# Optimization experiments

Hardware: AMD Instinct MI355X
Metric: run time of the kernel (lower is better)

Reference implementation:

```python
import jax, jax.numpy as jnp
import numpy as np

B, K, NPROP, NSAMPLE = 16, 2048, 256, 16
C_SEED, C_MLP = 256, 128
RADIUS = 0.3
NH, NSC, NCLS = 12, 18, 18
KZ, KXY, KLINE = 1024, 1024, 1024
SURF_TH, UP_TH = 0.5, 10.0
OUT_CH = 2 + 3 + 2 * NH + 4 * NSC + NCLS  # 119


def setup_inputs():
    key = jax.random.key(0)
    ks = iter(jax.random.split(key, 64))
    nrm = lambda shape, sc=1.0: sc * jax.random.normal(next(ks), shape, jnp.float32)
    uni = lambda shape: jax.random.uniform(next(ks), shape, jnp.float32, minval=-2.0, maxval=2.0)
    inp = {
        'vote_xyz': uni((B, K, 3)),
        'vote_features': nrm((B, C_SEED, K)),
        'pred_sem_class_z': nrm((B, 2, KZ)),
        'center_z': uni((B, KZ, 3)),
        'aggregated_feature_z': nrm((B, 128, KZ)),
        'pred_sem_class_xy': nrm((B, 2, KXY)),
        'center_xy': uni((B, KXY, 3)),
        'aggregated_feature_xy': nrm((B, 128, KXY)),
        'pred_sem_class_line': nrm((B, 2, KLINE)),
        'center_line': uni((B, KLINE, 3)),
        'aggregated_feature_line': nrm((B, 128, KLINE)),
        'mean_size_arr': jnp.abs(nrm((NSC, 3))) * 0.5 + 0.3,
        'mlp_w0': nrm((C_MLP, C_SEED + 3), 0.05),
        'mlp_s0': 1.0 + nrm((C_MLP,), 0.02),
        'mlp_b0': nrm((C_MLP,), 0.02),
        'mlp_w1': nrm((C_MLP, C_MLP), 0.05),
        'mlp_s1': 1.0 + nrm((C_MLP,), 0.02),
        'mlp_b1': nrm((C_MLP,), 0.02),
        'mlp_w2': nrm((C_MLP, C_MLP), 0.05),
        'mlp_s2': 1.0 + nrm((C_MLP,), 0.02),
        'mlp_b2': nrm((C_MLP,), 0.02),
        'conv1_w': nrm((C_MLP, C_MLP), 0.05),
        'conv1_b': nrm((C_MLP,), 0.02),
        'bn1_s': 1.0 + nrm((C_MLP,), 0.02),
        'bn1_b': nrm((C_MLP,), 0.02),
        'conv2_w': nrm((C_MLP, C_MLP), 0.05),
        'conv2_b': nrm((C_MLP,), 0.02),
        'bn2_s': 1.0 + nrm((C_MLP,), 0.02),
        'bn2_b': nrm((C_MLP,), 0.02),
        'conv3_w': nrm((OUT_CH, C_MLP), 0.05),
        'conv3_b': nrm((OUT_CH,), 0.02),
    }
    return inp


def fps(xyz, npoint):
    # furthest point sampling; xyz (B,N,3) -> (B,npoint) int32
    Bn, N, _ = xyz.shape
    bidx = jnp.arange(Bn)

    def step(carry, _):
        dist, far = carry
        centroid = xyz[bidx, far][:, None, :]  # (B,1,3)
        d = jnp.sum((xyz - centroid) ** 2, -1)
        dist = jnp.minimum(dist, d)
        nxt = jnp.argmax(dist, -1).astype(jnp.int32)
        return (dist, nxt), far

    init = (jnp.full((Bn, N), 1e10, xyz.dtype), jnp.zeros((Bn,), jnp.int32))
    _, inds = jax.lax.scan(step, init, None, length=npoint)
    return inds.T


def ball_group(xyz, feat_t, new_xyz, radius, nsample):
    # first-nsample-in-ball semantics (as CUDA ball_query), pad with first hit
    Bn, N, _ = xyz.shape
    d2 = jnp.sum((new_xyz[:, :, None] - xyz[:, None]) ** 2, -1)  # (B,P,N)
    score = jnp.where(d2 <= radius * radius, jnp.arange(N, dtype=jnp.int32), N)
    neg, idx = jax.lax.top_k(-score, nsample)
    idx = jnp.where(-neg < N, idx, idx[..., :1])
    b = jnp.arange(Bn)[:, None, None]
    gx = (xyz[b, idx] - new_xyz[:, :, None]) / radius  # normalize_xyz=True
    gf = feat_t[b, idx]
    return jnp.concatenate([gx, gf], -1)  # (B,P,ns,3+C)


def reference(vote_xyz, vote_features, pred_sem_class_z, center_z, aggregated_feature_z,
              pred_sem_class_xy, center_xy, aggregated_feature_xy,
              pred_sem_class_line, center_line, aggregated_feature_line, mean_size_arr,
              mlp_w0, mlp_s0, mlp_b0, mlp_w1, mlp_s1, mlp_b1, mlp_w2, mlp_s2, mlp_b2,
              conv1_w, conv1_b, bn1_s, bn1_b, conv2_w, conv2_b, bn2_s, bn2_b, conv3_w, conv3_b):
    # --- vote aggregation (PointnetSAModuleVotes, vote_fps) ---
    fps_inds = fps(vote_xyz, NPROP)
    bi = jnp.arange(vote_xyz.shape[0])[:, None]
    new_xyz = vote_xyz[bi, fps_inds]  # (B,P,3)
    g = ball_group(vote_xyz, vote_features.transpose(0, 2, 1), new_xyz, RADIUS, NSAMPLE)
    for w, s, b in ((mlp_w0, mlp_s0, mlp_b0), (mlp_w1, mlp_s1, mlp_b1), (mlp_w2, mlp_s2, mlp_b2)):
        g = jax.nn.relu(jnp.einsum('bpsc,oc->bpso', g, w) * s + b)  # conv2d 1x1 + folded BN + relu
    features = g.max(axis=2).transpose(0, 2, 1)  # (B,128,P)

    c1d = lambda x, w, b: jnp.einsum('bck,oc->bok', x, w) + b[None, :, None]
    bn = lambda x, s, b: x * s[None, :, None] + b[None, :, None]

    net = jax.nn.relu(bn(c1d(features, conv1_w, conv1_b), bn1_s, bn1_b))
    net = jax.nn.relu(bn(c1d(net, conv2_w, conv2_b), bn2_s, bn2_b))
    net = c1d(net, conv3_w, conv3_b)  # (B,119,P)

    # --- decode_scores (mode='center', start=2) ---
    nt = net.transpose(0, 2, 1)
    Bn, P = nt.shape[0], nt.shape[1]
    objectness = nt[..., 0:2]
    center = new_xyz + nt[..., 2:5]
    heading_scores = nt[..., 5:5 + NH]
    heading_res = nt[..., 5 + NH:5 + 2 * NH] * (np.pi / NH)
    size_scores = nt[..., 5 + 2 * NH:5 + 2 * NH + NSC]
    srn = nt[..., 5 + 2 * NH + NSC:5 + 2 * NH + 4 * NSC].reshape(Bn, P, NSC, 3)
    size_res = srn * mean_size_arr[None, None]
    sem_cls = nt[..., 5 + 2 * NH + 4 * NSC:]

    # --- surface / line center selection ---
    def sel_center(pred_sem, c):
        p = jax.nn.softmax(pred_sem, axis=1)
        sel = jax.lax.stop_gradient((p[:, 1, :] <= SURF_TH).astype(c.dtype))
        return c + UP_TH * sel[..., None]

    z_center = sel_center(pred_sem_class_z, center_z)
    xy_center = sel_center(pred_sem_class_xy, center_xy)
    line_center = sel_center(pred_sem_class_line, center_line)
    surface_center_pred = jnp.concatenate([z_center, xy_center], axis=1)
    surface_center_feature_pred = jnp.concatenate([aggregated_feature_z, aggregated_feature_xy], axis=2)

    # --- predicted box size -> 6 object surface centers ---
    cls = jnp.argmax(size_scores, -1)  # (B,P)
    pred_res = jnp.take_along_axis(size_res, cls[..., None, None], axis=2)[:, :, 0]
    pred_avg = mean_size_arr[cls]
    obj_size = jax.lax.stop_gradient(pred_avg + pred_res)  # .detach() in torch
    half = obj_size / 2.0
    z0 = jnp.zeros_like(half[..., :1])
    ez = jnp.concatenate([z0, z0, half[..., 2:3]], -1)
    ey = jnp.concatenate([z0, half[..., 1:2], z0], -1)
    ex = jnp.concatenate([half[..., 0:1], z0, z0], -1)
    obj_surface_center = jnp.concatenate([center + ez, center - ez, center + ey,
                                          center - ey, center + ex, center - ex], axis=1)
    obj_surface_feature = jnp.tile(features, (1, 1, 6))

    return (objectness, center, heading_scores, heading_res, size_scores, size_res, sem_cls,
            surface_center_pred, surface_center_feature_pred, line_center,
            obj_surface_center, obj_surface_feature)
```

## Files before the change

### kernel.cpp

```cpp
#include <hip/hip_runtime.h>

#define BB 16
#define KK 2048
#define NPROPN 256
#define NS 16
#define CSEED 256
#define CMLP 128
#define CIN 259
#define OUTCH 119
#define KZZ 1024

#define O0  0UL
#define O1  8192UL
#define O2  20480UL
#define O3  69632UL
#define O4  118784UL
#define O5  192512UL
#define O6  413696UL
#define O7  487424UL
#define O8  585728UL
#define O9  4780032UL
#define O10 4829184UL
#define O11 4902912UL

#define WS_NEWXYZ 0
#define WS_W0T 12288
#define WS_W1T 45440
#define WS_W2T 61824
#define WS_C1T 78208
#define WS_C2T 94592
#define WS_C3T 110976
#define WS_FEATT 131072UL
#define WS_NEED_BYTES ((size_t)(WS_FEATT + (size_t)BB * KK * CSEED) * 4)

#define XROWS 131
#define XSTR (XROWS * 16)

#define RSTEP(CTRL)                                                                          \
  {                                                                                          \
    unsigned shi = (unsigned)__builtin_amdgcn_update_dpp((int)hi, (int)hi, (CTRL), 0xF, 0xF, false); \
    unsigned slo = (unsigned)__builtin_amdgcn_update_dpp((int)lo, (int)lo, (CTRL), 0xF, 0xF, false); \
    bool gt = (shi > hi) || ((shi == hi) && (slo > lo));                                     \
    hi = gt ? shi : hi;                                                                      \
    lo = gt ? slo : lo;                                                                      \
  }

__device__ __forceinline__ void fma4(float4& a, float s, const float4& w) {
  a.x = fmaf(s, w.x, a.x); a.y = fmaf(s, w.y, a.y);
  a.z = fmaf(s, w.z, a.z); a.w = fmaf(s, w.w, a.w);
}
__device__ __forceinline__ float fget(const float4& v, int r) {
  return r == 0 ? v.x : (r == 1 ? v.y : (r == 2 ? v.z : v.w));
}
__device__ __forceinline__ int xadr(int row, int s4) {
  return row * 16 + (((s4) ^ ((row >> 2) & 3)) << 2);
}

template<bool TR>
__global__ __launch_bounds__(256) void prep_kernel(
    const float* __restrict__ xyz, const float* __restrict__ vote_feat,
    const float* __restrict__ w0, const float* __restrict__ w1, const float* __restrict__ w2,
    const float* __restrict__ c1w, const float* __restrict__ c2w, const float* __restrict__ c3w,
    const float* __restrict__ pz, const float* __restrict__ cz,
    const float* __restrict__ pxy, const float* __restrict__ cxy,
    const float* __restrict__ pl, const float* __restrict__ cl,
    const float* __restrict__ az, const float* __restrict__ axy,
    float* __restrict__ wsf, float* __restrict__ out) {
  constexpr int FPS_END = 16;
  constexpr int FEATT_END = FPS_END + (TR ? 1024 : 0);
  constexpr int TRW_END = FEATT_END + 450;
  constexpr int SURF_END = TRW_END + 192;

  const int bid = blockIdx.x;
  const int t = threadIdx.x;
  __shared__ float smem[8448];
  __shared__ unsigned fhi[2][4], flo[2][4];

  if (bid < FPS_END) {
    const int b = bid;
    const float* p = xyz + (size_t)b * KK * 3;
    float* sxyz = smem;
    float* nxb = smem + 6144;
    const int lane = t & 63, w = t >> 6;
    float pxr[8], pyr[8], pzr[8], dd[8];
#pragma unroll
    for (int j = 0; j < 8; ++j) {
      int i = j * 256 + t;
      float x = p[i * 3 + 0], y = p[i * 3 + 1], z = p[i * 3 + 2];
      pxr[j] = x; pyr[j] = y; pzr[j] = z; dd[j] = 1e10f;
      sxyz[i * 3 + 0] = x; sxyz[i * 3 + 1] = y; sxyz[i * 3 + 2] = z;
    }
    __syncthreads();
    int cur = 0;
    for (int it = 0; it < NPROPN; ++it) {
      const int pb = it & 1;
      float cx = sxyz[cur * 3 + 0];
      float cy = sxyz[cur * 3 + 1];
      float cz2 = sxyz[cur * 3 + 2];
      if (t == 0) { nxb[it * 3 + 0] = cx; nxb[it * 3 + 1] = cy; nxb[it * 3 + 2] = cz2; }
      float best = -1.0f;
      int bidx = 0;
#pragma unroll
      for (int j = 0; j < 8; ++j) {
        float dx = __fsub_rn(pxr[j], cx);
        float dy = __fsub_rn(pyr[j], cy);
        float dz = __fsub_rn(pzr[j], cz2);
        float d = __fadd_rn(__fadd_rn(__fmul_rn(dx, dx), __fmul_rn(dy, dy)), __fmul_rn(dz, dz));
        float nd = fminf(dd[j], d);
        dd[j] = nd;
        if (nd > best) { best = nd; bidx = j * 256 + t; }
      }
      unsigned hi = __float_as_uint(best);
      unsigned lo = ~(unsigned)bidx;
      RSTEP(0x111) RSTEP(0x112) RSTEP(0x114) RSTEP(0x118)
      RSTEP(0x142) RSTEP(0x143)
      if (lane == 63) { fhi[pb][w] = hi; flo[pb][w] = lo; }
      __syncthreads();
      unsigned vh = fhi[pb][0], vl = flo[pb][0];
#pragma unroll
      for (int q2 = 1; q2 < 4; ++q2) {
        unsigned ah = fhi[pb][q2], al = flo[pb][q2];
        bool gt = (ah > vh) || ((ah == vh) && (al > vl));
        vh = gt ? ah : vh; vl = gt ? al : vl;
      }
      cur = (int)~vl;
    }
    __syncthreads();
    float* nxw = wsf + WS_NEWXYZ + (size_t)b * NPROPN * 3;
    for (int i = t; i < NPROPN * 3; i += 256) nxw[i] = nxb[i];
    return;
  }

  if (TR && bid < FEATT_END) {
    int q = bid - FPS_END;
    int b = q >> 6, ck = q & 63;
    int k0 = ck << 5;
    float* tile = smem;
    const float* src = vote_feat + ((size_t)b * CSEED + t) * KK + k0;
    float4 v[8];
#pragma unroll
    for (int j = 0; j < 8; ++j) v[j] = *(const float4*)(src + j * 4);
#pragma unroll
    for (int j = 0; j < 8; ++j) {
      tile[(j * 4 + 0) * 260 + t] = v[j].x;
      tile[(j * 4 + 1) * 260 + t] = v[j].y;
      tile[(j * 4 + 2) * 260 + t] = v[j].z;
      tile[(j * 4 + 3) * 260 + t] = v[j].w;
    }
    __syncthreads();
    float* dst = wsf + WS_FEATT + ((size_t)b * KK + k0) * CSEED;
    const int kk = t >> 3, cbase = (t & 7) << 2;
#pragma unroll
    for (int j = 0; j < 8; ++j) {
      int c = cbase + (j << 5);
      float4 u = make_float4(tile[kk * 260 + c], tile[kk * 260 + c + 1],
                             tile[kk * 260 + c + 2], tile[kk * 260 + c + 3]);
      *(float4*)(dst + (size_t)kk * CSEED + c) = u;
    }
    return;
  }

  if (bid < TRW_END) {
    int row = (bid - FEATT_END) * 2 + (t >> 7);
    int o = t & 127;
    if (row < 899) {
      float v; float* dst;
      if (row < 259)      { dst = wsf + WS_W0T + (size_t)row * 128; v = w0[(size_t)o * CIN + row]; }
      else if (row < 387) { int k = row - 259; dst = wsf + WS_W1T + (size_t)k * 128; v = w1[(size_t)o * 128 + k]; }
      else if (row < 515) { int k = row - 387; dst = wsf + WS_W2T + (size_t)k * 128; v = w2[(size_t)o * 128 + k]; }
      else if (row < 643) { int k = row - 515; dst = wsf + WS_C1T + (size_t)k * 128; v = c1w[(size_t)o * 128 + k]; }
      else if (row < 771) { int k = row - 643; dst = wsf + WS_C2T + (size_t)k * 128; v = c2w[(size_t)o * 128 + k]; }
      else                { int k = row - 771; dst = wsf + WS_C3T + (size_t)k * 128; v = (o < OUTCH) ? c3w[(size_t)o * 128 + k] : 0.f; }
      dst[o] = v;
    }
    return;
  }

  if (bid < SURF_END) {
    int i = (bid - TRW_END) * 256 + t;
    int src = i / (BB * KZZ);
    int rem = i % (BB * KZZ);
    int b = rem / KZZ, k = rem % KZZ;
    const float* ps = (src == 0) ? pz : ((src == 1) ? pxy : pl);
    const float* pc = (src == 0) ? cz : ((src == 1) ? cxy : cl);
    float x0 = ps[((size_t)b * 2 + 0) * KZZ + k];
    float x1 = ps[((size_t)b * 2 + 1) * KZZ + k];
    float add = (x1 <= x0) ? 10.0f : 0.0f;
    size_t dst;
    if (src == 0)      dst = O7 + ((size_t)b * 2048 + k) * 3;
    else if (src == 1) dst = O7 + ((size_t)b * 2048 + 1024 + k) * 3;
    else               dst = O9 + ((size_t)b * KZZ + k) * 3;
    const float* c3 = pc + ((size_t)b * KZZ + k) * 3;
    out[dst + 0] = c3[0] + add;
    out[dst + 1] = c3[1] + add;
    out[dst + 2] = c3[2] + add;
    return;
  }

  {
    int i = (bid - SURF_END) * 256 + t;
    int q = i & 511;
    int bc = i >> 9;
    int half = q >> 8, k4 = q & 255;
    const float4* src = (const float4*)((half == 0) ? az : axy);
    float4 v = src[(size_t)bc * 256 + k4];
    float4* dst = (float4*)(out + O8);
    dst[(size_t)bc * 512 + q] = v;
  }
}

__device__ __forceinline__ void mlp_accum(const float* __restrict__ WT, int og, int sh,
                                          const float* __restrict__ xb, int K, float4* acc) {
  const float4* wp = (const float4*)WT + og;
  const int s4a = sh * 2, s4b = sh * 2 + 1;
#pragma unroll 4
  for (int k = 0; k < K; ++k) {
    float4 xa = *(const float4*)(xb + xadr(k, s4a));
    float4 xq = *(const float4*)(xb + xadr(k, s4b));
    float4 wv = wp[(size_t)k * 32];
    fma4(acc[0], xa.x, wv); fma4(acc[1], xa.y, wv);
    fma4(acc[2], xa.z, wv); fma4(acc[3], xa.w, wv);
    fma4(acc[4], xq.x, wv); fma4(acc[5], xq.y, wv);
    fma4(acc[6], xq.z, wv); fma4(acc[7], xq.w, wv);
  }
}

__device__ __forceinline__ void mlp_storeh(const float* __restrict__ scv, const float* __restrict__ bbv,
                                           int og, int sh, float* __restrict__ xb,
                                           const float4* __restrict__ acc) {
  float4 s4v = *(const float4*)(scv + (og << 2));
  float4 b4v = *(const float4*)(bbv + (og << 2));
#pragma unroll
  for (int r = 0; r < 4; ++r) {
    float ss = fget(s4v, r), bv = fget(b4v, r);
    float4 lo, hi;
    lo.x = fmaf(fget(acc[0], r), ss, bv); lo.x = lo.x > 0.f ? lo.x : 0.f;
    lo.y = fmaf(fget(acc[1], r), ss, bv); lo.y = lo.y > 0.f ? lo.y : 0.f;
    lo.z = fmaf(fget(acc[2], r), ss, bv); lo.z = lo.z > 0.f ? lo.z : 0.f;
    lo.w = fmaf(fget(acc[3], r), ss, bv); lo.w = lo.w > 0.f ? lo.w : 0.f;
    hi.x = fmaf(fget(acc[4], r), ss, bv); hi.x = hi.x > 0.f ? hi.x : 0.f;
    hi.y = fmaf(fget(acc[5], r), ss, bv); hi.y = hi.y > 0.f ? hi.y : 0.f;
    hi.z = fmaf(fget(acc[6], r), ss, bv); hi.z = hi.z > 0.f ? hi.z : 0.f;
    hi.w = fmaf(fget(acc[7], r), ss, bv); hi.w = hi.w > 0.f ? hi.w : 0.f;
    int row = (og << 2) + r;
    *(float4*)(xb + xadr(row, sh * 2)) = lo;
    *(float4*)(xb + xadr(row, sh * 2 + 1)) = hi;
  }
}

template<bool TR>
__global__ __launch_bounds__(256, 3) void proposal_kernel(
    const float* __restrict__ vote_xyz, const float* __restrict__ vote_feat,
    const float* __restrict__ wsf, const float* __restrict__ msa,
    const float* __restrict__ s0, const float* __restrict__ b0,
    const float* __restrict__ s1, const float* __restrict__ b1,
    const float* __restrict__ s2, const float* __restrict__ b2,
    const float* __restrict__ c1b, const float* __restrict__ bn1s, const float* __restrict__ bn1b,
    const float* __restrict__ c2b, const float* __restrict__ bn2s, const float* __restrict__ bn2b,
    const float* __restrict__ c3b,
    float* __restrict__ out) {
  __shared__ __align__(16) float Xbuf[4 * XSTR];
  __shared__ int sel_s[4][NS];
  __shared__ float feat_s[4][CMLP];
  __shared__ float n1_s[4][CMLP], n2_s[4][CMLP], ntv_s[4][CMLP];
  __shared__ float sc_s[4][3], sh_s[4][3];
  __shared__ int scls_s[4];

  const int t = threadIdx.x;
  const int w = t >> 6, l = t & 63;
  const int b = blockIdx.x >> 6;
  const int pp = ((blockIdx.x & 63) << 2) + w;
  const int sh = l >> 5, og = l & 31;
  float* Xw = Xbuf + w * XSTR;

  const float* nx = wsf + WS_NEWXYZ + ((size_t)b * NPROPN + pp) * 3;
  const float cx = nx[0], cy = nx[1], cz = nx[2];
  const float* px = vote_xyz + (size_t)b * KK * 3;
  const float RR = 0.09000000357627869f;

  {
    int total = 0;
    for (int j = 0; j < 32; ++j) {
      int i = (j << 6) + l;
      float dx = __fsub_rn(px[i * 3 + 0], cx);
      float dy = __fsub_rn(px[i * 3 + 1], cy);
      float dz = __fsub_rn(px[i * 3 + 2], cz);
      float d = __fadd_rn(__fadd_rn(__fmul_rn(dx, dx), __fmul_rn(dy, dy)), __fmul_rn(dz, dz));
      bool in = (d <= RR);
      unsigned long long bal = __ballot(in);
      if (in) {
        int pos = total + __popcll(bal & ((1ull << l) - 1ull));
        if (pos < NS) sel_s[w][pos] = i;
      }
      total += __popcll(bal);
      if (total >= NS) break;
    }
    if (l == 0 && total < NS) {
      int first = (total > 0) ? sel_s[w][0] : 0;
      for (int i = total; i < NS; ++i) sel_s[w][i] = first;
    }
    __builtin_amdgcn_wave_barrier();
  }

  float4 pf[8];
  {
    const int s = l >> 2, q = l & 3;
    const int idx = sel_s[w][s];
    const int s4 = s >> 2, se = s & 3;
    if (q < 3) {
      float pv = px[idx * 3 + q];
      float cv = (q == 0) ? cx : ((q == 1) ? cy : cz);
      Xw[xadr(q, s4) + se] = __fdiv_rn(__fsub_rn(pv, cv), 0.3f);
    }
    if constexpr (TR) {
      const float* fr = wsf + WS_FEATT + ((size_t)b * KK + idx) * CSEED;
#pragma unroll
      for (int m = 0; m < 8; ++m) {
        int c = (m << 4) + (q << 2);
        float4 v = *(const float4*)(fr + c);
        Xw[xadr(3 + c + 0, s4) + se] = v.x;
        Xw[xadr(3 + c + 1, s4) + se] = v.y;
        Xw[xadr(3 + c + 2, s4) + se] = v.z;
        Xw[xadr(3 + c + 3, s4) + se] = v.w;
      }
#pragma unroll
      for (int m = 0; m < 8; ++m) pf[m] = *(const float4*)(fr + 128 + (m << 4) + (q << 2));
    } else {
      const float* fb = vote_feat + (size_t)b * CSEED * KK + idx;
#pragma unroll
      for (int m = 0; m < 8; ++m) {
        int c = (m << 4) + (q << 2);
        Xw[xadr(3 + c + 0, s4) + se] = fb[(size_t)(c + 0) * KK];
        Xw[xadr(3 + c + 1, s4) + se] = fb[(size_t)(c + 1) * KK];
        Xw[xadr(3 + c + 2, s4) + se] = fb[(size_t)(c + 2) * KK];
        Xw[xadr(3 + c + 3, s4) + se] = fb[(size_t)(c + 3) * KK];
      }
#pragma unroll
      for (int m = 0; m < 8; ++m) {
        int c = 128 + (m << 4) + (q << 2);
        pf[m].x = fb[(size_t)(c + 0) * KK];
        pf[m].y = fb[(size_t)(c + 1) * KK];
        pf[m].z = fb[(size_t)(c + 2) * KK];
        pf[m].w = fb[(size_t)(c + 3) * KK];
      }
    }
    __builtin_amdgcn_wave_barrier();
  }

  float4 acc[8];
#pragma unroll
  for (int i = 0; i < 8; ++i) acc[i] = make_float4(0.f, 0.f, 0.f, 0.f);

  mlp_accum(wsf + WS_W0T, og, sh, Xw, 131, acc);
  __builtin_amdgcn_wave_barrier();

  {
    const int s = l >> 2, q = l & 3;
    const int s4 = s >> 2, se = s & 3;
#pragma unroll
    for (int m = 0; m < 8; ++m) {
      int c = (m << 4) + (q << 2);
      Xw[xadr(c + 0, s4) + se] = pf[m].x;
      Xw[xadr(c + 1, s4) + se] = pf[m].y;
      Xw[xadr(c + 2, s4) + se] = pf[m].z;
      Xw[xadr(c + 3, s4) + se] = pf[m].w;
    }
    __builtin_amdgcn_wave_barrier();
  }

  mlp_accum(wsf + WS_W0T + 131 * 128, og, sh, Xw, 128, acc);
  mlp_storeh(s0, b0, og, sh, Xw, acc);
  __builtin_amdgcn_wave_barrier();

#pragma unroll
  for (int i = 0; i < 8; ++i) acc[i] = make_float4(0.f, 0.f, 0.f, 0.f);
  mlp_accum(wsf + WS_W1T, og, sh, Xw, 128, acc);
  mlp_storeh(s1, b1, og, sh, Xw, acc);
  __builtin_amdgcn_wave_barrier();

#pragma unroll
  for (int i = 0; i < 8; ++i) acc[i] = make_float4(0.f, 0.f, 0.f, 0.f);
  mlp_accum(wsf + WS_W2T, og, sh, Xw, 128, acc);

  float mr[4];
  {
    float4 s4v = *(const float4*)(s2 + (og << 2));
    float4 b4v = *(const float4*)(b2 + (og << 2));
#pragma unroll
    for (int r = 0; r < 4; ++r) {
      float ss = fget(s4v, r), bv = fget(b4v, r);
      float m = 0.f;
#pragma unroll
      for (int i = 0; i < 8; ++i) m = fmaxf(m, fmaf(fget(acc[i], r), ss, bv));
      mr[r] = fmaxf(m, __shfl_xor(m, 32));
    }
  }
  if (sh == 0) *(float4*)&feat_s[w][og << 2] = make_float4(mr[0], mr[1], mr[2], mr[3]);
  __builtin_amdgcn_wave_barrier();

  {
    float* o11 = out + O11 + (size_t)b * CMLP * 1536;
#pragma unroll
    for (int r = 0; r < 4; ++r) {
      size_t rowb = (size_t)((og << 2) + r) * 1536 + pp;
#pragma unroll
      for (int rr2 = 0; rr2 < 3; ++rr2) {
        int rr = sh * 3 + rr2;
        o11[rowb + rr * 256] = mr[r];
      }
    }
  }

  {
    const float* C1T = wsf + WS_C1T;
    float a0 = 0.f, a1 = 0.f;
#pragma unroll 4
    for (int k = 0; k < CMLP; ++k) {
      float f = feat_s[w][k];
      float2 wv = *(const float2*)(C1T + (size_t)k * 128 + (l << 1));
      a0 = fmaf(f, wv.x, a0); a1 = fmaf(f, wv.y, a1);
    }
    int o0 = l << 1, o1 = o0 + 1;
    float v0 = fmaf(a0 + c1b[o0], bn1s[o0], bn1b[o0]); v0 = v0 > 0.f ? v0 : 0.f;
    float v1 = fmaf(a1 + c1b[o1], bn1s[o1], bn1b[o1]); v1 = v1 > 0.f ? v1 : 0.f;
    *(float2*)&n1_s[w][o0] = make_float2(v0, v1);
    __builtin_amdgcn_wave_barrier();
  }
  {
    const float* C2T = wsf + WS_C2T;
    float a0 = 0.f, a1 = 0.f;
#pragma unroll 4
    for (int k = 0; k < CMLP; ++k) {
      float f = n1_s[w][k];
      float2 wv = *(const float2*)(C2T + (size_t)k * 128 + (l << 1));
      a0 = fmaf(f, wv.x, a0); a1 = fmaf(f, wv.y, a1);
    }
    int o0 = l << 1, o1 = o0 + 1;
    float v0 = fmaf(a0 + c2b[o0], bn2s[o0], bn2b[o0]); v0 = v0 > 0.f ? v0 : 0.f;
    float v1 = fmaf(a1 + c2b[o1], bn2s[o1], bn2b[o1]); v1 = v1 > 0.f ? v1 : 0.f;
    *(float2*)&n2_s[w][o0] = make_float2(v0, v1);
    __builtin_amdgcn_wave_barrier();
  }
  {
    const float* C3T = wsf + WS_C3T;
    float a0 = 0.f, a1 = 0.f;
#pragma unroll 4
    for (int k = 0; k < CMLP; ++k) {
      float f = n2_s[w][k];
      float2 wv = *(const float2*)(C3T + (size_t)k * 128 + (l << 1));
      a0 = fmaf(f, wv.x, a0); a1 = fmaf(f, wv.y, a1);
    }
    int o0 = l << 1, o1 = o0 + 1;
    float bb0 = (o0 < OUTCH) ? c3b[o0] : 0.f;
    float bb1 = (o1 < OUTCH) ? c3b[o1] : 0.f;
    *(float2*)&ntv_s[w][o0] = make_float2(a0 + bb0, a1 + bb1);
    __builtin_amdgcn_wave_barrier();
  }

  {
    const float* ntv = &ntv_s[w][0];
    const size_t bp = (size_t)b * NPROPN + pp;
    if (l < 2) out[O0 + bp * 2 + l] = ntv[l];
    if (l < 3) {
      float cv = ((l == 0) ? cx : ((l == 1) ? cy : cz)) + ntv[2 + l];
      sc_s[w][l] = cv;
      out[O1 + bp * 3 + l] = cv;
    }
    if (l < 12) {
      out[O2 + bp * 12 + l] = ntv[5 + l];
      out[O3 + bp * 12 + l] = ntv[17 + l] * 0.2617993877991494f;
    }
    if (l < 18) {
      out[O4 + bp * 18 + l] = ntv[29 + l];
      out[O6 + bp * 18 + l] = ntv[101 + l];
    }
    if (l < 54) out[O5 + bp * 54 + l] = ntv[47 + l] * msa[l];
    if (l == 0) {
      float bvv = ntv[29]; int bii = 0;
      for (int i2 = 1; i2 < 18; ++i2)
        if (ntv[29 + i2] > bvv) { bvv = ntv[29 + i2]; bii = i2; }
      scls_s[w] = bii;
    }
    __builtin_amdgcn_wave_barrier();
    if (l < 3) {
      int cls = scls_s[w];
      float m = msa[cls * 3 + l];
      sh_s[w][l] = fmaf(ntv[47 + cls * 3 + l], m, m) * 0.5f;
    }
    __builtin_amdgcn_wave_barrier();
    if (l < 18) {
      const int r = l / 3, j2 = l % 3;
      const int axis[6] = {2, 2, 1, 1, 0, 0};
      float v = sc_s[w][j2];
      if (j2 == axis[r]) v = (r & 1) ? (v - sh_s[w][j2]) : (v + sh_s[w][j2]);
      out[O10 + (size_t)b * 4608 + (size_t)(r * 256 + pp) * 3 + j2] = v;
    }
  }
}

extern "C" void kernel_launch(void* const* d_in, const int* in_sizes, int n_in,
                              void* d_out, int out_size, void* d_ws, size_t ws_size,
                              hipStream_t stream) {
  (void)in_sizes; (void)n_in; (void)out_size;
  const float* vote_xyz = (const float*)d_in[0];
  const float* vote_feat = (const float*)d_in[1];
  const float* pz   = (const float*)d_in[2];
  const float* cz   = (const float*)d_in[3];
  const float* az   = (const float*)d_in[4];
  const float* pxy  = (const float*)d_in[5];
  const float* cxy  = (const float*)d_in[6];
  const float* axy  = (const float*)d_in[7];
  const float* pl   = (const float*)d_in[8];
  const float* cl   = (const float*)d_in[9];
  const float* msa  = (const float*)d_in[11];
  const float* w0   = (const float*)d_in[12];
  const float* s0   = (const float*)d_in[13];
  const float* b0   = (const float*)d_in[14];
  const float* w1   = (const float*)d_in[15];
  const float* s1   = (const float*)d_in[16];
  const float* b1   = (const float*)d_in[17];
  const float* w2   = (const float*)d_in[18];
  const float* s2   = (const float*)d_in[19];
  const float* b2   = (const float*)d_in[20];
  const float* c1w  = (const float*)d_in[21];
  const float* c1b  = (const float*)d_in[22];
  const float* bn1s = (const float*)d_in[23];
  const float* bn1b = (const float*)d_in[24];
  const float* c2w  = (const float*)d_in[25];
  const float* c2b  = (const float*)d_in[26];
  const float* bn2s = (const float*)d_in[27];
  const float* bn2b = (const float*)d_in[28];
  const float* c3w  = (const float*)d_in[29];
  const float* c3b  = (const float*)d_in[30];
  float* out = (float*)d_out;
  float* wsf = (float*)d_ws;

  if (ws_size >= WS_NEED_BYTES) {
    hipLaunchKernelGGL((prep_kernel<true>), dim3(16 + 1024 + 450 + 192 + 4096), dim3(256), 0, stream,
                       vote_xyz, vote_feat, w0, w1, w2, c1w, c2w, c3w,
                       pz, cz, pxy, cxy, pl, cl, az, axy, wsf, out);
    hipLaunchKernelGGL((proposal_kernel<true>), dim3(BB * NPROPN / 4), dim3(256), 0, stream,
                       vote_xyz, vote_feat, wsf, msa,
                       s0, b0, s1, b1, s2, b2,
                       c1b, bn1s, bn1b, c2b, bn2s, bn2b, c3b, out);
  } else {
    hipLaunchKernelGGL((prep_kernel<false>), dim3(16 + 450 + 192 + 4096), dim3(256), 0, stream,
                       vote_xyz, vote_feat, w0, w1, w2, c1w, c2w, c3w,
                       pz, cz, pxy, cxy, pl, cl, az, axy, wsf, out);
    hipLaunchKernelGGL((proposal_kernel<false>), dim3(BB * NPROPN / 4), dim3(256), 0, stream,
                       vote_xyz, vote_feat, wsf, msa,
                       s0, b0, s1, b1, s2, b2,
                       c1b, bn1s, bn1b, c2b, bn2s, bn2b, c3b, out);
  }
}
```

Baseline: 377.3 us.

## Carry FPS winner coordinates through DPP reduction and alias proposal scratch into Xbuf

Measured after the change: 379.9 us. Within noise of the previous version (+0.7%).

```diff
diff --git a/kernel.cpp b/kernel.cpp
--- a/kernel.cpp
+++ b/kernel.cpp
@@ -36,13 +36,16 @@
 #define XROWS 131
 #define XSTR (XROWS * 16)
 
-#define RSTEP(CTRL)                                                                          \
-  {                                                                                          \
+#define RSTEP5(CTRL)                                                                           \
+  {                                                                                            \
     unsigned shi = (unsigned)__builtin_amdgcn_update_dpp((int)hi, (int)hi, (CTRL), 0xF, 0xF, false); \
     unsigned slo = (unsigned)__builtin_amdgcn_update_dpp((int)lo, (int)lo, (CTRL), 0xF, 0xF, false); \
-    bool gt = (shi > hi) || ((shi == hi) && (slo > lo));                                     \
-    hi = gt ? shi : hi;                                                                      \
-    lo = gt ? slo : lo;                                                                      \
+    unsigned sx  = (unsigned)__builtin_amdgcn_update_dpp((int)bx, (int)bx, (CTRL), 0xF, 0xF, false); \
+    unsigned sy  = (unsigned)__builtin_amdgcn_update_dpp((int)by, (int)by, (CTRL), 0xF, 0xF, false); \
+    unsigned sz  = (unsigned)__builtin_amdgcn_update_dpp((int)bz, (int)bz, (CTRL), 0xF, 0xF, false); \
+    bool gt = (shi > hi) || ((shi == hi) && (slo > lo));                                       \
+    hi = gt ? shi : hi; lo = gt ? slo : lo;                                                    \
+    bx = gt ? sx : bx;  by = gt ? sy : by;  bz = gt ? sz : bz;                                 \
   }
 
 __device__ __forceinline__ void fma4(float4& a, float s, const float4& w) {
@@ -74,56 +77,67 @@
   const int bid = blockIdx.x;
   const int t = threadIdx.x;
   __shared__ float smem[8448];
-  __shared__ unsigned fhi[2][4], flo[2][4];
+  __shared__ __align__(16) unsigned fres[2][5][4];
 
   if (bid < FPS_END) {
     const int b = bid;
     const float* p = xyz + (size_t)b * KK * 3;
-    float* sxyz = smem;
-    float* nxb = smem + 6144;
+    float* nxb = smem;
     const int lane = t & 63, w = t >> 6;
     float pxr[8], pyr[8], pzr[8], dd[8];
 #pragma unroll
     for (int j = 0; j < 8; ++j) {
       int i = j * 256 + t;
-      float x = p[i * 3 + 0], y = p[i * 3 + 1], z = p[i * 3 + 2];
-      pxr[j] = x; pyr[j] = y; pzr[j] = z; dd[j] = 1e10f;
-      sxyz[i * 3 + 0] = x; sxyz[i * 3 + 1] = y; sxyz[i * 3 + 2] = z;
-    }
-    __syncthreads();
-    int cur = 0;
+      pxr[j] = p[i * 3 + 0]; pyr[j] = p[i * 3 + 1]; pzr[j] = p[i * 3 + 2];
+      dd[j] = 1e10f;
+    }
+    float ccx = p[0], ccy = p[1], ccz = p[2];
     for (int it = 0; it < NPROPN; ++it) {
       const int pb = it & 1;
-      float cx = sxyz[cur * 3 + 0];
-      float cy = sxyz[cur * 3 + 1];
-      float cz2 = sxyz[cur * 3 + 2];
-      if (t == 0) { nxb[it * 3 + 0] = cx; nxb[it * 3 + 1] = cy; nxb[it * 3 + 2] = cz2; }
+      if (t == 0) { nxb[it * 3 + 0] = ccx; nxb[it * 3 + 1] = ccy; nxb[it * 3 + 2] = ccz; }
       float best = -1.0f;
-      int bidx = 0;
+      int bj = 0;
 #pragma unroll
       for (int j = 0; j < 8; ++j) {
-        float dx = __fsub_rn(pxr[j], cx);
-        float dy = __fsub_rn(pyr[j], cy);
-        float dz = __fsub_rn(pzr[j], cz2);
+        float dx = __fsub_rn(pxr[j], ccx);
+        float dy = __fsub_rn(pyr[j], ccy);
+        float dz = __fsub_rn(pzr[j], ccz);
         float d = __fadd_rn(__fadd_rn(__fmul_rn(dx, dx), __fmul_rn(dy, dy)), __fmul_rn(dz, dz));
         float nd = fminf(dd[j], d);
         dd[j] = nd;
-        if (nd > best) { best = nd; bidx = j * 256 + t; }
+        if (nd > best) { best = nd; bj = j; }
+      }
+      float fx = pxr[0], fy = pyr[0], fz = pzr[0];
+#pragma unroll
+      for (int j = 1; j < 8; ++j) {
+        bool e = (bj == j);
+        fx = e ? pxr[j] : fx; fy = e ? pyr[j] : fy; fz = e ? pzr[j] : fz;
       }
       unsigned hi = __float_as_uint(best);
-      unsigned lo = ~(unsigned)bidx;
-      RSTEP(0x111) RSTEP(0x112) RSTEP(0x114) RSTEP(0x118)
-      RSTEP(0x142) RSTEP(0x143)
-      if (lane == 63) { fhi[pb][w] = hi; flo[pb][w] = lo; }
+      unsigned lo = ~(unsigned)((bj << 8) + t);
+      unsigned bx = __float_as_uint(fx), by = __float_as_uint(fy), bz = __float_as_uint(fz);
+      RSTEP5(0x111) RSTEP5(0x112) RSTEP5(0x114) RSTEP5(0x118)
+      RSTEP5(0x142) RSTEP5(0x143)
+      if (lane == 63) {
+        fres[pb][0][w] = hi; fres[pb][1][w] = lo;
+        fres[pb][2][w] = bx; fres[pb][3][w] = by; fres[pb][4][w] = bz;
+      }
       __syncthreads();
-      unsigned vh = fhi[pb][0], vl = flo[pb][0];
-#pragma unroll
-      for (int q2 = 1; q2 < 4; ++q2) {
-        unsigned ah = fhi[pb][q2], al = flo[pb][q2];
-        bool gt = (ah > vh) || ((ah == vh) && (al > vl));
-        vh = gt ? ah : vh; vl = gt ? al : vl;
-      }
-      cur = (int)~vl;
+      uint4 H = *(const uint4*)&fres[pb][0][0];
+      uint4 L = *(const uint4*)&fres[pb][1][0];
+      uint4 X = *(const uint4*)&fres[pb][2][0];
+      uint4 Y = *(const uint4*)&fres[pb][3][0];
+      uint4 Z = *(const uint4*)&fres[pb][4][0];
+      unsigned vh = H.x, vl = L.x, vx = X.x, vy = Y.x, vz = Z.x;
+      {
+        bool g1 = (H.y > vh) || ((H.y == vh) && (L.y > vl));
+        vh = g1 ? H.y : vh; vl = g1 ? L.y : vl; vx = g1 ? X.y : vx; vy = g1 ? Y.y : vy; vz = g1 ? Z.y : vz;
+        bool g2 = (H.z > vh) || ((H.z == vh) && (L.z > vl));
+        vh = g2 ? H.z : vh; vl = g2 ? L.z : vl; vx = g2 ? X.z : vx; vy = g2 ? Y.z : vy; vz = g2 ? Z.z : vz;
+        bool g3 = (H.w > vh) || ((H.w == vh) && (L.w > vl));
+        vh = g3 ? H.w : vh; vl = g3 ? L.w : vl; vx = g3 ? X.w : vx; vy = g3 ? Y.w : vy; vz = g3 ? Z.w : vz;
+      }
+      ccx = __uint_as_float(vx); ccy = __uint_as_float(vy); ccz = __uint_as_float(vz);
     }
     __syncthreads();
     float* nxw = wsf + WS_NEWXYZ + (size_t)b * NPROPN * 3;
@@ -249,7 +263,7 @@
 }
 
 template<bool TR>
-__global__ __launch_bounds__(256, 3) void proposal_kernel(
+__global__ __launch_bounds__(256, 4) void proposal_kernel(
     const float* __restrict__ vote_xyz, const float* __restrict__ vote_feat,
     const float* __restrict__ wsf, const float* __restrict__ msa,
     const float* __restrict__ s0, const float* __restrict__ b0,
@@ -261,8 +275,6 @@
     float* __restrict__ out) {
   __shared__ __align__(16) float Xbuf[4 * XSTR];
   __shared__ int sel_s[4][NS];
-  __shared__ float feat_s[4][CMLP];
-  __shared__ float n1_s[4][CMLP], n2_s[4][CMLP], ntv_s[4][CMLP];
   __shared__ float sc_s[4][3], sh_s[4][3];
   __shared__ int scls_s[4];
 
@@ -272,6 +284,10 @@
   const int pp = ((blockIdx.x & 63) << 2) + w;
   const int sh = l >> 5, og = l & 31;
   float* Xw = Xbuf + w * XSTR;
+  float* feat_p = Xw;
+  float* n1_p   = Xw + 128;
+  float* n2_p   = Xw + 256;
+  float* ntv_p  = Xw + 384;
 
   const float* nx = wsf + WS_NEWXYZ + ((size_t)b * NPROPN + pp) * 3;
   const float cx = nx[0], cy = nx[1], cz = nx[2];
@@ -395,7 +411,8 @@
       mr[r] = fmaxf(m, __shfl_xor(m, 32));
     }
   }
-  if (sh == 0) *(float4*)&feat_s[w][og << 2] = make_float4(mr[0], mr[1], mr[2], mr[3]);
+  __builtin_amdgcn_wave_barrier();
+  if (sh == 0) *(float4*)(feat_p + (og << 2)) = make_float4(mr[0], mr[1], mr[2], mr[3]);
   __builtin_amdgcn_wave_barrier();
 
   {
@@ -416,14 +433,14 @@
     float a0 = 0.f, a1 = 0.f;
 #pragma unroll 4
     for (int k = 0; k < CMLP; ++k) {
-      float f = feat_s[w][k];
+      float f = feat_p[k];
       float2 wv = *(const float2*)(C1T + (size_t)k * 128 + (l << 1));
       a0 = fmaf(f, wv.x, a0); a1 = fmaf(f, wv.y, a1);
     }
     int o0 = l << 1, o1 = o0 + 1;
     float v0 = fmaf(a0 + c1b[o0], bn1s[o0], bn1b[o0]); v0 = v0 > 0.f ? v0 : 0.f;
     float v1 = fmaf(a1 + c1b[o1], bn1s[o1], bn1b[o1]); v1 = v1 > 0.f ? v1 : 0.f;
-    *(float2*)&n1_s[w][o0] = make_float2(v0, v1);
+    *(float2*)(n1_p + o0) = make_float2(v0, v1);
     __builtin_amdgcn_wave_barrier();
   }
   {
@@ -431,14 +448,14 @@
     float a0 = 0.f, a1 = 0.f;
 #pragma unroll 4
     for (int k = 0; k < CMLP; ++k) {
-      float f = n1_s[w][k];
+      float f = n1_p[k];
       float2 wv = *(const float2*)(C2T + (size_t)k * 128 + (l << 1));
       a0 = fmaf(f, wv.x, a0); a1 = fmaf(f, wv.y, a1);
     }
     int o0 = l << 1, o1 = o0 + 1;
     float v0 = fmaf(a0 + c2b[o0], bn2s[o0], bn2b[o0]); v0 = v0 > 0.f ? v0 : 0.f;
     float v1 = fmaf(a1 + c2b[o1], bn2s[o1], bn2b[o1]); v1 = v1 > 0.f ? v1 : 0.f;
-    *(float2*)&n2_s[w][o0] = make_float2(v0, v1);
+    *(float2*)(n2_p + o0) = make_float2(v0, v1);
     __builtin_amdgcn_wave_barrier();
   }
   {
@@ -446,46 +463,45 @@
     float a0 = 0.f, a1 = 0.f;
 #pragma unroll 4
     for (int k = 0; k < CMLP; ++k) {
-      float f = n2_s[w][k];
+      float f = n2_p[k];
       float2 wv = *(const float2*)(C3T + (size_t)k * 128 + (l << 1));
       a0 = fmaf(f, wv.x, a0); a1 = fmaf(f, wv.y, a1);
     }
     int o0 = l << 1, o1 = o0 + 1;
     float bb0 = (o0 < OUTCH) ? c3b[o0] : 0.f;
     float bb1 = (o1 < OUTCH) ? c3b[o1] : 0.f;
-    *(float2*)&ntv_s[w][o0] = make_float2(a0 + bb0, a1 + bb1);
-    __builtin_amdgcn_wave_barrier();
-  }
-
-  {
-    const float* ntv = &ntv_s[w][0];
+    *(float2*)(ntv_p + o0) = make_float2(a0 + bb0, a1 + bb1);
+    __builtin_amdgcn_wave_barrier();
+  }
+
+  {
     const size_t bp = (size_t)b * NPROPN + pp;
-    if (l < 2) out[O0 + bp * 2 + l] = ntv[l];
+    if (l < 2) out[O0 + bp * 2 + l] = ntv_p[l];
     if (l < 3) {
-      float cv = ((l == 0) ? cx : ((l == 1) ? cy : cz)) + ntv[2 + l];
+      float cv = ((l == 0) ? cx : ((l == 1) ? cy : cz)) + ntv_p[2 + l];
       sc_s[w][l] = cv;
       out[O1 + bp * 3 + l] = cv;
     }
     if (l < 12) {
-      out[O2 + bp * 12 + l] = ntv[5 + l];
-      out[O3 + bp * 12 + l] = ntv[17 + l] * 0.2617993877991494f;
+      out[O2 + bp * 12 + l] = ntv_p[5 + l];
+      out[O3 + bp * 12 + l] = ntv_p[17 + l] * 0.2617993877991494f;
     }
     if (l < 18) {
-      out[O4 + bp * 18 + l] = ntv[29 + l];
-      out[O6 + bp * 18 + l] = ntv[101 + l];
-    }
-    if (l < 54) out[O5 + bp * 54 + l] = ntv[47 + l] * msa[l];
+      out[O4 + bp * 18 + l] = ntv_p[29 + l];
+      out[O6 + bp * 18 + l] = ntv_p[101 + l];
+    }
+    if (l < 54) out[O5 + bp * 54 + l] = ntv_p[47 + l] * msa[l];
     if (l == 0) {
-      float bvv = ntv[29]; int bii = 0;
+      float bvv = ntv_p[29]; int bii = 0;
       for (int i2 = 1; i2 < 18; ++i2)
-        if (ntv[29 + i2] > bvv) { bvv = ntv[29 + i2]; bii = i2; }
+        if (ntv_p[29 + i2] > bvv) { bvv = ntv_p[29 + i2]; bii = i2; }
       scls_s[w] = bii;
     }
     __builtin_amdgcn_wave_barrier();
     if (l < 3) {
       int cls = scls_s[w];
       float m = msa[cls * 3 + l];
-      sh_s[w][l] = fmaf(ntv[47 + cls * 3 + l], m, m) * 0.5f;
+      sh_s[w][l] = fmaf(ntv_p[47 + cls * 3 + l], m, m) * 0.5f;
     }
     __builtin_amdgcn_wave_barrier();
     if (l < 18) {
```
